# Kernel optimization log

Measured on AMD Instinct MI355X. Metric: run time of the kernel, lower is better.

## Reference

```python
import jax, jax.numpy as jnp
import numpy as np

B = 262144
HIST = 24
FORE = 20
HID = 256
# torch: tau_int = clamp(tau,1,18).long().item(); default tau=6.0 -> static 6 (host sync in torch)
TAU_INT = 6


def setup_inputs() -> dict:
    key = jax.random.key(0)
    ks = jax.random.split(key, 9)
    s = 0.1
    return {
        "history": jax.random.normal(ks[0], (B, HIST), jnp.float32),
        "enc_w1": jax.random.normal(ks[1], (HIST + FORE, HID), jnp.float32) * s,
        "enc_b1": jnp.zeros((HID,), jnp.float32),
        "enc_w2": jax.random.normal(ks[2], (HID, HID), jnp.float32) * s,
        "enc_b2": jnp.zeros((HID,), jnp.float32),
        "cor_w1": jax.random.normal(ks[3], (HID, HID), jnp.float32) * s,
        "cor_b1": jnp.zeros((HID,), jnp.float32),
        "cor_w2": jax.random.normal(ks[4], (HID, FORE), jnp.float32) * s,
        "cor_b2": jnp.zeros((FORE,), jnp.float32),
        "alpha": jnp.float32(0.2),
        "beta": jnp.float32(0.3),
        "gamma": jnp.float32(0.01),
        "tau": jnp.float32(6.0),
        "lambda_mix": jnp.float32(0.5),
    }


def _physics_core(history, alpha, beta, gamma, steps):
    a = jax.nn.sigmoid(alpha)
    b = jax.nn.sigmoid(beta)
    g = jnp.abs(gamma)
    T0 = history[:, -1]                      # [B]
    buf0 = history[:, -TAU_INT:].T           # [tau, B]; buf0[0] = history[:, -tau]

    def step(carry, _):
        T, buf = carry
        T_delayed = buf[0]
        T_new = T - a * T - b * T_delayed - g * T ** 3
        buf = jnp.concatenate([buf[1:], T_new[None, :]], axis=0)
        return (T_new, buf), T_new

    _, preds = jax.lax.scan(step, (T0, buf0), None, length=steps)
    return preds.T                            # [B, steps]


def reference(history, enc_w1, enc_b1, enc_w2, enc_b2,
              cor_w1, cor_b1, cor_w2, cor_b2,
              alpha, beta, gamma, tau, lambda_mix):
    T_physics = _physics_core(history, alpha, beta, gamma, FORE)   # [B, FORE]
    combined = jnp.concatenate([history, T_physics], axis=1)       # [B, HIST+FORE]
    h = jnp.tanh(combined @ enc_w1 + enc_b1)
    features = jnp.tanh(h @ enc_w2 + enc_b2)
    c = jnp.tanh(features @ cor_w1 + cor_b1)
    T_soft = c @ cor_w2 + cor_b2                                   # [B, FORE]
    lam = jax.nn.sigmoid(lambda_mix)
    T_pred = T_physics + lam * T_soft
    return (T_pred, T_physics, T_soft)
```

## Files before the change

### kernel.cpp

```cpp
#include <hip/hip_runtime.h>
#include <hip/hip_bf16.h>

#define NROWS 262144
#define HISTC 24
#define FOREC 20

typedef __bf16        v8bf __attribute__((ext_vector_type(8)));
typedef float         v4f  __attribute__((ext_vector_type(4)));
typedef float         v2f  __attribute__((ext_vector_type(2)));
typedef unsigned int  v4u  __attribute__((ext_vector_type(4)));
typedef unsigned int  v2u  __attribute__((ext_vector_type(2)));

#define WS_WT1_OFF 64
#define WT1_ELEMS 16384
#define WT2_ELEMS 65536
#define WT3_ELEMS 65536
#define WT4R_ELEMS 65536

#define TANH_C 2.885390081777927f

__device__ __forceinline__ unsigned short f2bf(float x) {
    unsigned u = __builtin_bit_cast(unsigned, x);
    u += 0x7FFFu + ((u >> 16) & 1u);
    return (unsigned short)(u >> 16);
}

__device__ __forceinline__ unsigned packbf2(float a, float b) {
    unsigned ua = __builtin_bit_cast(unsigned, a) + 0x8000u;
    unsigned ub = __builtin_bit_cast(unsigned, b) + 0x8000u;
    return __builtin_amdgcn_perm(ub, ua, 0x07060302u);
}

__device__ __forceinline__ void lds_barrier() {
    asm volatile("s_waitcnt lgkmcnt(0)\n\ts_barrier" ::: "memory");
}

__device__ __forceinline__ int swzi(int r, int byteoff) {
    return (r << 8) + (((byteoff) ^ ((r & 7) << 4)) >> 1);
}

__global__ void prep_kernel(const float* __restrict__ w1, const float* __restrict__ w2,
                            const float* __restrict__ w3, const float* __restrict__ w4,
                            const float* __restrict__ alpha, const float* __restrict__ beta,
                            const float* __restrict__ gamma, const float* __restrict__ lmix,
                            unsigned char* __restrict__ ws)
{
    if (blockIdx.x == 104) {
        int t = threadIdx.x;
        float* wsf = (float*)ws;
        if (t == 0) wsf[0] = 1.0f / (1.0f + expf(-alpha[0]));
        else if (t == 1) wsf[1] = 1.0f / (1.0f + expf(-beta[0]));
        else if (t == 2) wsf[2] = fabsf(gamma[0]);
        else if (t == 3) wsf[3] = 1.0f / (1.0f + expf(-lmix[0]));
        return;
    }
    int idx = (blockIdx.x * 256 + threadIdx.x) * 8;
    const float* src;
    int KT, Kreal, Nreal, srcN, local, ntmask;
    unsigned short* dst = (unsigned short*)(ws + WS_WT1_OFF);
    if (idx < WT1_ELEMS) {
        local = idx; src = w1; KT = 2; Kreal = 44; Nreal = 256; srcN = 256; ntmask = 255;
    } else if (idx < WT1_ELEMS + WT2_ELEMS) {
        local = idx - WT1_ELEMS; dst += WT1_ELEMS;
        src = w2; KT = 8; Kreal = 256; Nreal = 256; srcN = 256; ntmask = 255;
    } else if (idx < WT1_ELEMS + WT2_ELEMS + WT3_ELEMS) {
        local = idx - (WT1_ELEMS + WT2_ELEMS); dst += WT1_ELEMS + WT2_ELEMS;
        src = w3; KT = 8; Kreal = 256; Nreal = 256; srcN = 256; ntmask = 255;
    } else {
        local = idx - (WT1_ELEMS + WT2_ELEMS + WT3_ELEMS);
        dst += WT1_ELEMS + WT2_ELEMS + WT3_ELEMS;
        src = w4; KT = 8; Kreal = 256; Nreal = 20; srcN = 20; ntmask = 1;
    }
    int L   = (local >> 3) & 63;
    int blk = local >> 9;
    int kt = blk % KT, nt = (blk / KT) & ntmask;
    int cc = L & 15,  qq = L >> 4;
    int feat = nt * 16 + cc;
    int kbase = kt * 32 + qq * 8;
    unsigned short tmp[8];
#pragma unroll
    for (int j = 0; j < 8; ++j) {
        int k = kbase + j;
        float v = (k < Kreal && feat < Nreal) ? src[k * srcN + feat] : 0.0f;
        tmp[j] = f2bf(v);
    }
    v4u pk;
    pk[0] = tmp[0] | ((unsigned)tmp[1] << 16);
    pk[1] = tmp[2] | ((unsigned)tmp[3] << 16);
    pk[2] = tmp[4] | ((unsigned)tmp[5] << 16);
    pk[3] = tmp[6] | ((unsigned)tmp[7] << 16);
    *(v4u*)&dst[local] = pk;
}

template<int KT, int KTN>
__device__ __forceinline__ void layer_pipe(unsigned short* buf,
        const v4u* __restrict__ wp, const v4u* __restrict__ wpn,
        const float* __restrict__ bias, v4u A[2][4],
        int w, int c, int q, int lane)
{
    v4f acc[4][4];
#pragma unroll
    for (int ft = 0; ft < 4; ++ft)
#pragma unroll
        for (int st = 0; st < 4; ++st) {
            v4f z = {0.0f, 0.0f, 0.0f, 0.0f};
            acc[ft][st] = z;
        }

#pragma unroll
    for (int kt = 0; kt < KT; ++kt) {
        const int cs = kt & 1;
        const int ps = cs ^ 1;
        if (kt + 1 < KT) {
#pragma unroll
            for (int ft = 0; ft < 4; ++ft)
                A[ps][ft] = wp[((w * 4 + ft) * KT + kt + 1) * 64 + lane];
        } else {
#pragma unroll
            for (int ft = 0; ft < 4; ++ft)
                A[ps][ft] = wpn[((w * 4 + ft) * KTN + 0) * 64 + lane];
        }
#pragma unroll
        for (int st = 0; st < 4; ++st) {
            v4u braw = *(const v4u*)&buf[swzi(st * 16 + c, kt * 64 + q * 16)];
            v8bf bb = __builtin_bit_cast(v8bf, braw);
#pragma unroll
            for (int ft = 0; ft < 4; ++ft)
                acc[ft][st] = __builtin_amdgcn_mfma_f32_16x16x32_bf16(
                    __builtin_bit_cast(v8bf, A[cs][ft]), bb, acc[ft][st], 0, 0, 0);
        }
    }

    lds_barrier();

#pragma unroll
    for (int ft = 0; ft < 4; ++ft) {
        v4f bi = *(const v4f*)&bias[w * 64 + ft * 16 + q * 4];
        v4f bic;
#pragma unroll
        for (int r = 0; r < 4; ++r) bic[r] = bi[r] * TANH_C;
#pragma unroll
        for (int st = 0; st < 4; ++st) {
            float x[4];
#pragma unroll
            for (int r = 0; r < 4; ++r) {
                float t = __builtin_fmaf(acc[ft][st][r], TANH_C, bic[r]);
                float p = __builtin_amdgcn_exp2f(t);
                float rc = __builtin_amdgcn_rcpf(p + 1.0f);
                x[r] = __builtin_fmaf(-2.0f, rc, 1.0f);
            }
            v2u d; d[0] = packbf2(x[0], x[1]); d[1] = packbf2(x[2], x[3]);
            *(v2u*)&buf[swzi(st * 16 + c, w * 128 + ft * 32 + q * 8)] = d;
        }
    }
    lds_barrier();
}

__global__ __launch_bounds__(256, 4) void fused_kernel(
    const float* __restrict__ history,
    const float* __restrict__ eb1, const float* __restrict__ eb2,
    const float* __restrict__ cb1, const float* __restrict__ cb2,
    const unsigned char* __restrict__ ws, float* __restrict__ out)
{
    __shared__ unsigned short buf[64 * 256];
    __shared__ float tp[64 * 20];

    const int tid  = threadIdx.x;
    const int w    = tid >> 6;
    const int lane = tid & 63;
    const int c    = lane & 15;
    const int q    = lane >> 4;
    const int row0 = blockIdx.x << 6;
    const float* wsf = (const float*)ws;
    const v4u* wp1 = (const v4u*)(ws + WS_WT1_OFF);
    const v4u* wp2 = wp1 + WT1_ELEMS / 8;
    const v4u* wp3 = wp2 + WT2_ELEMS / 8;
    const v4u* wp4 = wp3 + WT3_ELEMS / 8;

    v4u A[2][4];
#pragma unroll
    for (int ft = 0; ft < 4; ++ft)
        A[0][ft] = wp1[((w * 4 + ft) * 2 + 0) * 64 + lane];

#pragma unroll
    for (int i = 0; i < 2; ++i) {
        int e = tid + i * 256;
        if (e < 384) {
            int r  = e / 6, c4 = e - r * 6;
            v4f h4 = *(const v4f*)&history[(long)(row0 + r) * 24 + c4 * 4];
            v2u d; d[0] = packbf2(h4[0], h4[1]); d[1] = packbf2(h4[2], h4[3]);
            *(v2u*)&buf[swzi(r, c4 * 8)] = d;
        }
    }
#pragma unroll
    for (int i = 0; i < 2; ++i) {
        int e = tid + i * 256;
        if (e < 320) {
            int r = e / 5, g = e - r * 5;
            v2u z = {0u, 0u};
            *(v2u*)&buf[swzi(r, 88 + g * 8)] = z;
        }
    }
    if (tid < 64) {
        const float* hrow = &history[(long)(row0 + tid) * 24];
        v2f h18 = *(const v2f*)&hrow[18];
        v4f h20 = *(const v4f*)&hrow[20];
        float pa = wsf[0], pb = wsf[1], pg = wsf[2];
        float d0 = h18[0], d1 = h18[1], d2 = h20[0];
        float d3 = h20[1], d4 = h20[2], d5 = h20[3];
        float T = d5;
#pragma unroll
        for (int s = 0; s < 20; ++s) {
            float t3 = T * T * T;
            float Tn = T - pa * T;
            Tn = Tn - pb * d0;
            Tn = Tn - pg * t3;
            tp[tid * 20 + s] = Tn;
            buf[swzi(tid, 48 + 2 * s)] = f2bf(Tn);
            d0 = d1; d1 = d2; d2 = d3; d3 = d4; d4 = d5; d5 = Tn;
            T = Tn;
        }
    }
    lds_barrier();

    layer_pipe<2, 8>(buf, wp1, wp2, eb1, A, w, c, q, lane);
    layer_pipe<8, 8>(buf, wp2, wp3, eb2, A, w, c, q, lane);
    layer_pipe<8, 8>(buf, wp3, wp4, cb1, A, w, c, q, lane);

    v4f acc40 = {0.0f, 0.0f, 0.0f, 0.0f}, acc41 = {0.0f, 0.0f, 0.0f, 0.0f};
#pragma unroll
    for (int kt = 0; kt < 8; ++kt) {
        const int cs = kt & 1, ps = cs ^ 1;
        if (kt + 1 < 8) {
            A[ps][0] = wp4[((w * 4 + 0) * 8 + kt + 1) * 64 + lane];
            A[ps][1] = wp4[((w * 4 + 1) * 8 + kt + 1) * 64 + lane];
        }
        v4u braw = *(const v4u*)&buf[swzi(w * 16 + c, kt * 64 + q * 16)];
        v8bf bb = __builtin_bit_cast(v8bf, braw);
        acc40 = __builtin_amdgcn_mfma_f32_16x16x32_bf16(
            __builtin_bit_cast(v8bf, A[cs][0]), bb, acc40, 0, 0, 0);
        acc41 = __builtin_amdgcn_mfma_f32_16x16x32_bf16(
            __builtin_bit_cast(v8bf, A[cs][1]), bb, acc41, 0, 0, 0);
    }

    const float lam = wsf[3];
    const long sample = (long)row0 + w * 16 + c;
    float* outP = out;
    float* outF = out + (long)NROWS * 20;
    float* outS = out + (long)NROWS * 40;
    {
        int f0 = q * 4;
        v4f bi  = *(const v4f*)&cb2[f0];
        v4f tph = *(const v4f*)&tp[(w * 16 + c) * 20 + f0];
        v4f ts, pr;
#pragma unroll
        for (int r = 0; r < 4; ++r) {
            ts[r] = acc40[r] + bi[r];
            pr[r] = tph[r] + lam * ts[r];
        }
        *(v4f*)&outS[sample * 20 + f0] = ts;
        *(v4f*)&outP[sample * 20 + f0] = pr;
        *(v4f*)&outF[sample * 20 + f0] = tph;
    }
    if (q == 0) {
        v4f bi  = *(const v4f*)&cb2[16];
        v4f tph = *(const v4f*)&tp[(w * 16 + c) * 20 + 16];
        v4f ts, pr;
#pragma unroll
        for (int r = 0; r < 4; ++r) {
            ts[r] = acc41[r] + bi[r];
            pr[r] = tph[r] + lam * ts[r];
        }
        *(v4f*)&outS[sample * 20 + 16] = ts;
        *(v4f*)&outP[sample * 20 + 16] = pr;
        *(v4f*)&outF[sample * 20 + 16] = tph;
    }
}

extern "C" void kernel_launch(void* const* d_in, const int* in_sizes, int n_in,
                              void* d_out, int out_size, void* d_ws, size_t ws_size,
                              hipStream_t stream)
{
    const float* history = (const float*)d_in[0];
    const float* enc_w1  = (const float*)d_in[1];
    const float* enc_b1  = (const float*)d_in[2];
    const float* enc_w2  = (const float*)d_in[3];
    const float* enc_b2  = (const float*)d_in[4];
    const float* cor_w1  = (const float*)d_in[5];
    const float* cor_b1  = (const float*)d_in[6];
    const float* cor_w2  = (const float*)d_in[7];
    const float* cor_b2  = (const float*)d_in[8];
    const float* alpha   = (const float*)d_in[9];
    const float* beta    = (const float*)d_in[10];
    const float* gamma   = (const float*)d_in[11];
    const float* lmix    = (const float*)d_in[13];

    prep_kernel<<<105, 256, 0, stream>>>(enc_w1, enc_w2, cor_w1, cor_w2,
                                         alpha, beta, gamma, lmix,
                                         (unsigned char*)d_ws);
    fused_kernel<<<NROWS / 64, 256, 0, stream>>>(history, enc_b1, enc_b2, cor_b1, cor_b2,
                                                 (const unsigned char*)d_ws, (float*)d_out);
}
```

Before: 201.7 us.

## Split each 64-row tile across eight waves instead of four

The fused MLP kernel now launches 512 threads per block, so each of eight waves computes 32 output features per layer instead of 64. This halves the accumulator and weight-register footprint per wave. In the final layer, pairs of waves split the two 16-feature output tiles. The aim is more waves in flight to hide latency. It depends on the weight prefetch layout (w*2+ft indexing) matching the prep kernel's packing, and it puts more waves behind each barrier.

New measurement: 199.7 us. About the same (-1.0%).

```diff
diff --git a/kernel.cpp b/kernel.cpp
--- a/kernel.cpp
+++ b/kernel.cpp
@@ -95,12 +95,12 @@
 template<int KT, int KTN>
 __device__ __forceinline__ void layer_pipe(unsigned short* buf,
         const v4u* __restrict__ wp, const v4u* __restrict__ wpn,
-        const float* __restrict__ bias, v4u A[2][4],
+        const float* __restrict__ bias, v4u A[2][2],
         int w, int c, int q, int lane)
 {
-    v4f acc[4][4];
-#pragma unroll
-    for (int ft = 0; ft < 4; ++ft)
+    v4f acc[2][4];
+#pragma unroll
+    for (int ft = 0; ft < 2; ++ft)
 #pragma unroll
         for (int st = 0; st < 4; ++st) {
             v4f z = {0.0f, 0.0f, 0.0f, 0.0f};
@@ -113,19 +113,19 @@
         const int ps = cs ^ 1;
         if (kt + 1 < KT) {
 #pragma unroll
-            for (int ft = 0; ft < 4; ++ft)
-                A[ps][ft] = wp[((w * 4 + ft) * KT + kt + 1) * 64 + lane];
+            for (int ft = 0; ft < 2; ++ft)
+                A[ps][ft] = wp[((w * 2 + ft) * KT + kt + 1) * 64 + lane];
         } else {
 #pragma unroll
-            for (int ft = 0; ft < 4; ++ft)
-                A[ps][ft] = wpn[((w * 4 + ft) * KTN + 0) * 64 + lane];
+            for (int ft = 0; ft < 2; ++ft)
+                A[ps][ft] = wpn[((w * 2 + ft) * KTN + 0) * 64 + lane];
         }
 #pragma unroll
         for (int st = 0; st < 4; ++st) {
             v4u braw = *(const v4u*)&buf[swzi(st * 16 + c, kt * 64 + q * 16)];
             v8bf bb = __builtin_bit_cast(v8bf, braw);
 #pragma unroll
-            for (int ft = 0; ft < 4; ++ft)
+            for (int ft = 0; ft < 2; ++ft)
                 acc[ft][st] = __builtin_amdgcn_mfma_f32_16x16x32_bf16(
                     __builtin_bit_cast(v8bf, A[cs][ft]), bb, acc[ft][st], 0, 0, 0);
         }
@@ -134,8 +134,8 @@
     lds_barrier();
 
 #pragma unroll
-    for (int ft = 0; ft < 4; ++ft) {
-        v4f bi = *(const v4f*)&bias[w * 64 + ft * 16 + q * 4];
+    for (int ft = 0; ft < 2; ++ft) {
+        v4f bi = *(const v4f*)&bias[w * 32 + ft * 16 + q * 4];
         v4f bic;
 #pragma unroll
         for (int r = 0; r < 4; ++r) bic[r] = bi[r] * TANH_C;
@@ -150,13 +150,13 @@
                 x[r] = __builtin_fmaf(-2.0f, rc, 1.0f);
             }
             v2u d; d[0] = packbf2(x[0], x[1]); d[1] = packbf2(x[2], x[3]);
-            *(v2u*)&buf[swzi(st * 16 + c, w * 128 + ft * 32 + q * 8)] = d;
+            *(v2u*)&buf[swzi(st * 16 + c, w * 64 + ft * 32 + q * 8)] = d;
         }
     }
     lds_barrier();
 }
 
-__global__ __launch_bounds__(256, 4) void fused_kernel(
+__global__ __launch_bounds__(512, 6) void fused_kernel(
     const float* __restrict__ history,
     const float* __restrict__ eb1, const float* __restrict__ eb2,
     const float* __restrict__ cb1, const float* __restrict__ cb2,
@@ -177,29 +177,21 @@
     const v4u* wp3 = wp2 + WT2_ELEMS / 8;
     const v4u* wp4 = wp3 + WT3_ELEMS / 8;
 
-    v4u A[2][4];
-#pragma unroll
-    for (int ft = 0; ft < 4; ++ft)
-        A[0][ft] = wp1[((w * 4 + ft) * 2 + 0) * 64 + lane];
-
-#pragma unroll
-    for (int i = 0; i < 2; ++i) {
-        int e = tid + i * 256;
-        if (e < 384) {
-            int r  = e / 6, c4 = e - r * 6;
-            v4f h4 = *(const v4f*)&history[(long)(row0 + r) * 24 + c4 * 4];
-            v2u d; d[0] = packbf2(h4[0], h4[1]); d[1] = packbf2(h4[2], h4[3]);
-            *(v2u*)&buf[swzi(r, c4 * 8)] = d;
-        }
-    }
-#pragma unroll
-    for (int i = 0; i < 2; ++i) {
-        int e = tid + i * 256;
-        if (e < 320) {
-            int r = e / 5, g = e - r * 5;
-            v2u z = {0u, 0u};
-            *(v2u*)&buf[swzi(r, 88 + g * 8)] = z;
-        }
+    v4u A[2][2];
+#pragma unroll
+    for (int ft = 0; ft < 2; ++ft)
+        A[0][ft] = wp1[((w * 2 + ft) * 2 + 0) * 64 + lane];
+
+    if (tid < 384) {
+        int r  = tid / 6, c4 = tid - r * 6;
+        v4f h4 = *(const v4f*)&history[(long)(row0 + r) * 24 + c4 * 4];
+        v2u d; d[0] = packbf2(h4[0], h4[1]); d[1] = packbf2(h4[2], h4[3]);
+        *(v2u*)&buf[swzi(r, c4 * 8)] = d;
+    }
+    if (tid < 320) {
+        int r = tid / 5, g = tid - r * 5;
+        v2u z = {0u, 0u};
+        *(v2u*)&buf[swzi(r, 88 + g * 8)] = z;
     }
     if (tid < 64) {
         const float* hrow = &history[(long)(row0 + tid) * 24];
@@ -227,48 +219,46 @@
     layer_pipe<8, 8>(buf, wp2, wp3, eb2, A, w, c, q, lane);
     layer_pipe<8, 8>(buf, wp3, wp4, cb1, A, w, c, q, lane);
 
-    v4f acc40 = {0.0f, 0.0f, 0.0f, 0.0f}, acc41 = {0.0f, 0.0f, 0.0f, 0.0f};
+    const int sw = w >> 1, fw = w & 1;
+    v4f acc4 = {0.0f, 0.0f, 0.0f, 0.0f};
+    v4u wa = fw ? A[0][1] : A[0][0];
 #pragma unroll
     for (int kt = 0; kt < 8; ++kt) {
-        const int cs = kt & 1, ps = cs ^ 1;
-        if (kt + 1 < 8) {
-            A[ps][0] = wp4[((w * 4 + 0) * 8 + kt + 1) * 64 + lane];
-            A[ps][1] = wp4[((w * 4 + 1) * 8 + kt + 1) * 64 + lane];
-        }
-        v4u braw = *(const v4u*)&buf[swzi(w * 16 + c, kt * 64 + q * 16)];
+        v4u wn;
+        if (kt + 1 < 8)
+            wn = wp4[((w * 2 + fw) * 8 + kt + 1) * 64 + lane];
+        v4u braw = *(const v4u*)&buf[swzi(sw * 16 + c, kt * 64 + q * 16)];
         v8bf bb = __builtin_bit_cast(v8bf, braw);
-        acc40 = __builtin_amdgcn_mfma_f32_16x16x32_bf16(
-            __builtin_bit_cast(v8bf, A[cs][0]), bb, acc40, 0, 0, 0);
-        acc41 = __builtin_amdgcn_mfma_f32_16x16x32_bf16(
-            __builtin_bit_cast(v8bf, A[cs][1]), bb, acc41, 0, 0, 0);
+        acc4 = __builtin_amdgcn_mfma_f32_16x16x32_bf16(
+            __builtin_bit_cast(v8bf, wa), bb, acc4, 0, 0, 0);
+        if (kt + 1 < 8) wa = wn;
     }
 
     const float lam = wsf[3];
-    const long sample = (long)row0 + w * 16 + c;
+    const long sample = (long)row0 + sw * 16 + c;
     float* outP = out;
     float* outF = out + (long)NROWS * 20;
     float* outS = out + (long)NROWS * 40;
-    {
+    if (fw == 0) {
         int f0 = q * 4;
         v4f bi  = *(const v4f*)&cb2[f0];
-        v4f tph = *(const v4f*)&tp[(w * 16 + c) * 20 + f0];
+        v4f tph = *(const v4f*)&tp[(sw * 16 + c) * 20 + f0];
         v4f ts, pr;
 #pragma unroll
         for (int r = 0; r < 4; ++r) {
-            ts[r] = acc40[r] + bi[r];
+            ts[r] = acc4[r] + bi[r];
             pr[r] = tph[r] + lam * ts[r];
         }
         *(v4f*)&outS[sample * 20 + f0] = ts;
         *(v4f*)&outP[sample * 20 + f0] = pr;
         *(v4f*)&outF[sample * 20 + f0] = tph;
-    }
-    if (q == 0) {
+    } else if (q == 0) {
         v4f bi  = *(const v4f*)&cb2[16];
-        v4f tph = *(const v4f*)&tp[(w * 16 + c) * 20 + 16];
+        v4f tph = *(const v4f*)&tp[(sw * 16 + c) * 20 + 16];
         v4f ts, pr;
 #pragma unroll
         for (int r = 0; r < 4; ++r) {
-            ts[r] = acc41[r] + bi[r];
+            ts[r] = acc4[r] + bi[r];
             pr[r] = tph[r] + lam * ts[r];
         }
         *(v4f*)&outS[sample * 20 + 16] = ts;
@@ -298,6 +288,6 @@
     prep_kernel<<<105, 256, 0, stream>>>(enc_w1, enc_w2, cor_w1, cor_w2,
                                          alpha, beta, gamma, lmix,
                                          (unsigned char*)d_ws);
-    fused_kernel<<<NROWS / 64, 256, 0, stream>>>(history, enc_b1, enc_b2, cor_b1, cor_b2,
+    fused_kernel<<<NROWS / 64, 512, 0, stream>>>(history, enc_b1, enc_b2, cor_b1, cor_b2,
                                                  (const unsigned char*)d_ws, (float*)d_out);
 }
```
